# Kernel optimization log

Hardware: AMD Instinct MI355X
Metric: run time of the kernel (lower is better)

## Reference

```python
import jax, jax.numpy as jnp
import numpy as np

B, T, V = 32, 100, 20000
E, H, M, DD = 128, 128, 64, 2


def setup_inputs() -> dict:
    key = jax.random.key(0)
    ks = jax.random.split(key, 12)
    x = jax.random.uniform(ks[0], (B, T, V), dtype=jnp.float32)
    # zero out trailing timesteps per example so Masking layer matters
    lens = jax.random.randint(ks[1], (B,), T * 3 // 4, T + 1)
    tmask = (jnp.arange(T)[None, :] < lens[:, None]).astype(jnp.float32)
    x = x * tmask[:, :, None]
    a = jax.random.uniform(ks[2], (B, V), dtype=jnp.float32)
    d = jax.random.normal(ks[3], (B, DD), dtype=jnp.float32)
    # parameters
    emb = jax.random.uniform(ks[4], (V, E), minval=-0.1, maxval=0.1, dtype=jnp.float32)
    s = 1.0 / np.sqrt(E)
    gru_k = jax.random.uniform(ks[5], (E, 3 * H), minval=-s, maxval=s, dtype=jnp.float32)
    gru_rk = jax.random.normal(ks[6], (H, 3 * H), dtype=jnp.float32) / np.sqrt(H)
    gru_b_i = jnp.zeros((3 * H,), jnp.float32)   # input bias (reset_after=True)
    gru_b_r = jnp.zeros((3 * H,), jnp.float32)   # recurrent bias
    s1 = 1.0 / np.sqrt(H + E)
    W1 = jax.random.uniform(ks[7], (H + E, M), minval=-s1, maxval=s1, dtype=jnp.float32)
    b1 = jnp.zeros((M,), jnp.float32)
    s2 = 1.0 / np.sqrt(M + DD)
    W2 = jax.random.uniform(ks[8], (M + DD, 1), minval=-s2, maxval=s2, dtype=jnp.float32)
    b2 = jnp.zeros((1,), jnp.float32)
    return dict(x=x, a=a, d=d, emb=emb, gru_k=gru_k, gru_rk=gru_rk,
                gru_b_i=gru_b_i, gru_b_r=gru_b_r, W1=W1, b1=b1, W2=W2, b2=b2)


def _gru_final_state(xe, mask, gru_k, gru_rk, gru_b_i, gru_b_r):
    # xe: [B,T,E], mask: [B,T] bool. Keras GRU, reset_after=True, eval mode (dropout off).
    Hn = gru_rk.shape[0]
    x_proj = jnp.einsum('bte,eh->bth', xe, gru_k) + gru_b_i  # [B,T,3H]

    def step(h, inp):
        xp_t, m_t = inp                      # [B,3H], [B]
        rec = h @ gru_rk + gru_b_r           # [B,3H]
        xz, xr, xh = jnp.split(xp_t, 3, axis=-1)
        rz, rr, rh = jnp.split(rec, 3, axis=-1)
        z = jax.nn.sigmoid(xz + rz)
        r = jax.nn.sigmoid(xr + rr)
        hh = jnp.tanh(xh + r * rh)
        h_new = z * h + (1.0 - z) * hh
        h = jnp.where(m_t[:, None], h_new, h)  # masked steps carry state
        return h, None

    h0 = jnp.zeros((xe.shape[0], Hn), xe.dtype)
    h_final, _ = jax.lax.scan(step, h0, (jnp.swapaxes(x_proj, 0, 1), jnp.swapaxes(mask, 0, 1)))
    return h_final


def reference(x, a, d, emb, gru_k, gru_rk, gru_b_i, gru_b_r, W1, b1, W2, b2):
    ae = jnp.tanh(a @ emb)                       # [B,E]
    xe = jnp.tanh(jnp.einsum('btv,ve->bte', x, emb))  # [B,T,E]
    mask = jnp.any(xe != 0.0, axis=-1)           # Masking(mask_value=0.0)
    h = _gru_final_state(xe, mask, gru_k, gru_rk, gru_b_i, gru_b_r)  # [B,H]
    c = jnp.tanh(jnp.concatenate([h, ae], axis=1) @ W1 + b1)         # [B,M]
    out = jax.nn.sigmoid(jnp.concatenate([c, d], axis=1) @ W2 + b2)  # [B,1]
    return out
```

## Files before the change

kernel.cpp:

```cpp
#include <hip/hip_runtime.h>

typedef __attribute__((ext_vector_type(8))) short short8;
typedef __attribute__((ext_vector_type(4))) float float4v;

#define V_ 20000
#define KS 8
#define ARS 264

__device__ __forceinline__ unsigned short f2bf(float f) {
    union { float f; unsigned int u; } v; v.f = f;
    unsigned int u = v.u;
    u += 0x7fffu + ((u >> 16) & 1u);
    return (unsigned short)(u >> 16);
}

__device__ __forceinline__ float fast_tanh(float x) {
    float xc = fminf(15.f, fmaxf(-15.f, x));
    float e = __expf(2.f * xc);
    return (e - 1.f) / (e + 1.f);
}

__device__ __forceinline__ float sigmoidf_(float x) {
    float xc = fminf(30.f, fmaxf(-30.f, x));
    return 1.f / (1.f + __expf(-xc));
}

__global__ __launch_bounds__(256) void cvt_embT(const float* __restrict__ emb,
                                                unsigned short* __restrict__ embT) {
    __shared__ unsigned short tile[128 * 65];
    int tid = threadIdx.x;
    int k0 = blockIdx.x * 64;
    const float4v* e4 = (const float4v*)emb;
    #pragma unroll
    for (int c = 0; c < 8; ++c) {
        int l4 = c * 256 + tid;
        int k = l4 >> 5;
        int n4 = l4 & 31;
        float4v f = {0.f, 0.f, 0.f, 0.f};
        if (k0 + k < V_) f = e4[(size_t)(k0 + k) * 32 + n4];
        tile[(n4 * 4 + 0) * 65 + k] = f2bf(f.x);
        tile[(n4 * 4 + 1) * 65 + k] = f2bf(f.y);
        tile[(n4 * 4 + 2) * 65 + k] = f2bf(f.z);
        tile[(n4 * 4 + 3) * 65 + k] = f2bf(f.w);
    }
    __syncthreads();
    #pragma unroll
    for (int c = 0; c < 4; ++c) {
        int l8 = c * 256 + tid;
        int n = l8 >> 3, seg = l8 & 7;
        int kk = k0 + seg * 8;
        if (kk < V_) {
            short8 v;
            #pragma unroll
            for (int i = 0; i < 8; ++i) v[i] = (short)tile[n * 65 + seg * 8 + i];
            *(short8*)(embT + (size_t)n * V_ + kk) = v;
        }
    }
}

__global__ __launch_bounds__(256) void big_gemm(const float* __restrict__ x,
                                                const float* __restrict__ a,
                                                const unsigned short* __restrict__ embT,
                                                float* __restrict__ partial) {
    __shared__ unsigned short Alds[2][16 * ARS];
    int tid = threadIdx.x;
    int bx = blockIdx.x, by = blockIdx.y;
    int m0 = bx * 16;
    const int per = 79 / KS, extra = 79 % KS;
    int sc0 = by * per + (by < extra ? by : extra);
    int nsc = per + (by < extra ? 1 : 0);

    int r = tid >> 4, c = tid & 15;
    int rg = m0 + r;
    const float* __restrict__ srcA = (rg < 3200) ? (x + (size_t)rg * V_)
                                                 : (a + (size_t)(rg - 3200) * V_);
    int lane = tid & 63, w = tid >> 6;
    int ln = lane & 15, quad = lane >> 4;
    const unsigned short* __restrict__ bb0 = embT + (size_t)(w * 32 + ln) * V_ + quad * 8;
    const unsigned short* __restrict__ bb1 = bb0 + (size_t)16 * V_;
    int aoff = ln * ARS + quad * 8;

    float4v acc0 = {0.f, 0.f, 0.f, 0.f}, acc1 = {0.f, 0.f, 0.f, 0.f};
    float4v p0, p1, p2, p3;

    {
        int k0 = sc0 * 256;
        int nkb = 625 - sc0 * 8; if (nkb > 8) nkb = 8;
        int L = nkb * 32;
        if (c * 16 < L) {
            const float4v* ap = (const float4v*)(srcA + k0 + c * 16);
            p0 = ap[0]; p1 = ap[1]; p2 = ap[2]; p3 = ap[3];
        } else {
            p0 = p1 = p2 = p3 = (float4v){0.f, 0.f, 0.f, 0.f};
        }
        short8 w0, w1;
        w0[0]=(short)f2bf(p0.x); w0[1]=(short)f2bf(p0.y); w0[2]=(short)f2bf(p0.z); w0[3]=(short)f2bf(p0.w);
        w0[4]=(short)f2bf(p1.x); w0[5]=(short)f2bf(p1.y); w0[6]=(short)f2bf(p1.z); w0[7]=(short)f2bf(p1.w);
        w1[0]=(short)f2bf(p2.x); w1[1]=(short)f2bf(p2.y); w1[2]=(short)f2bf(p2.z); w1[3]=(short)f2bf(p2.w);
        w1[4]=(short)f2bf(p3.x); w1[5]=(short)f2bf(p3.y); w1[6]=(short)f2bf(p3.z); w1[7]=(short)f2bf(p3.w);
        *(short8*)&Alds[0][r * ARS + c * 16]     = w0;
        *(short8*)&Alds[0][r * ARS + c * 16 + 8] = w1;
    }
    __syncthreads();

    for (int s = 0; s < nsc; ++s) {
        int buf = s & 1;
        int sc = sc0 + s;
        int k0 = sc * 256;
        int nkb = 625 - sc * 8; if (nkb > 8) nkb = 8;
        bool more = (s + 1 < nsc);
        if (more) {
            int k0n = (sc + 1) * 256;
            int nkbn = 625 - (sc + 1) * 8; if (nkbn > 8) nkbn = 8;
            if (c * 16 < nkbn * 32) {
                const float4v* ap = (const float4v*)(srcA + k0n + c * 16);
                p0 = ap[0]; p1 = ap[1]; p2 = ap[2]; p3 = ap[3];
            } else {
                p0 = p1 = p2 = p3 = (float4v){0.f, 0.f, 0.f, 0.f};
            }
        }
        const unsigned short* bp0 = bb0 + k0;
        const unsigned short* bp1 = bb1 + k0;
        const unsigned short* al = &Alds[buf][aoff];
        if (nkb == 8) {
            #pragma unroll
            for (int kk = 0; kk < 8; ++kk) {
                short8 af = *(const short8*)(al + kk * 32);
                short8 f0 = *(const short8*)(bp0 + kk * 32);
                short8 f1 = *(const short8*)(bp1 + kk * 32);
                acc0 = __builtin_amdgcn_mfma_f32_16x16x32_bf16(af, f0, acc0, 0, 0, 0);
                acc1 = __builtin_amdgcn_mfma_f32_16x16x32_bf16(af, f1, acc1, 0, 0, 0);
            }
        } else {
            for (int kk = 0; kk < nkb; ++kk) {
                short8 af = *(const short8*)(al + kk * 32);
                short8 f0 = *(const short8*)(bp0 + kk * 32);
                short8 f1 = *(const short8*)(bp1 + kk * 32);
                acc0 = __builtin_amdgcn_mfma_f32_16x16x32_bf16(af, f0, acc0, 0, 0, 0);
                acc1 = __builtin_amdgcn_mfma_f32_16x16x32_bf16(af, f1, acc1, 0, 0, 0);
            }
        }
        if (more) {
            int nxt = buf ^ 1;
            short8 w0, w1;
            w0[0]=(short)f2bf(p0.x); w0[1]=(short)f2bf(p0.y); w0[2]=(short)f2bf(p0.z); w0[3]=(short)f2bf(p0.w);
            w0[4]=(short)f2bf(p1.x); w0[5]=(short)f2bf(p1.y); w0[6]=(short)f2bf(p1.z); w0[7]=(short)f2bf(p1.w);
            w1[0]=(short)f2bf(p2.x); w1[1]=(short)f2bf(p2.y); w1[2]=(short)f2bf(p2.z); w1[3]=(short)f2bf(p2.w);
            w1[4]=(short)f2bf(p3.x); w1[5]=(short)f2bf(p3.y); w1[6]=(short)f2bf(p3.z); w1[7]=(short)f2bf(p3.w);
            *(short8*)&Alds[nxt][r * ARS + c * 16]     = w0;
            *(short8*)&Alds[nxt][r * ARS + c * 16 + 8] = w1;
        }
        __syncthreads();
    }

    size_t base = ((size_t)by * 3232 + m0 + quad * 4) * 128 + w * 32 + ln;
    #pragma unroll
    for (int reg = 0; reg < 4; ++reg) {
        partial[base + (size_t)reg * 128]      = acc0[reg];
        partial[base + (size_t)reg * 128 + 16] = acc1[reg];
    }
}

__global__ __launch_bounds__(128) void reduce_tanh(const float* __restrict__ partial,
                                                   float* __restrict__ xe,
                                                   float* __restrict__ ae,
                                                   float* __restrict__ maskg) {
    int row = blockIdx.x;
    int e = threadIdx.x;
    float s = 0.f;
    #pragma unroll
    for (int k = 0; k < KS; ++k)
        s += partial[((size_t)k * 3232 + row) * 128 + e];
    float v = fast_tanh(s);
    if (row < 3200) {
        xe[(size_t)row * 128 + e] = v;
        __shared__ int any;
        if (e == 0) any = 0;
        __syncthreads();
        if (v != 0.f) any = 1;
        __syncthreads();
        if (e == 0) maskg[row] = any ? 1.f : 0.f;
    } else {
        ae[(row - 3200) * 128 + e] = v;
    }
}

__global__ __launch_bounds__(384) void xproj_kernel(const float* __restrict__ xe,
                                                    const float* __restrict__ gru_k,
                                                    const float* __restrict__ b_i,
                                                    float* __restrict__ xproj) {
    __shared__ float xs[16 * 128];
    int tid = threadIdx.x;
    int row0 = blockIdx.x * 16;
    const float4v* src = (const float4v*)(xe + (size_t)row0 * 128);
    float4v* dstl = (float4v*)xs;
    #pragma unroll
    for (int c = 0; c < 2; ++c) {
        int i4 = c * 384 + tid;
        if (i4 < 512) dstl[i4] = src[i4];
    }
    __syncthreads();
    int j = tid;
    float acc[16];
    #pragma unroll
    for (int r = 0; r < 16; ++r) acc[r] = 0.f;
    float bi = b_i[j];
    for (int k4 = 0; k4 < 32; ++k4) {
        float g0 = gru_k[(k4 * 4 + 0) * 384 + j];
        float g1 = gru_k[(k4 * 4 + 1) * 384 + j];
        float g2 = gru_k[(k4 * 4 + 2) * 384 + j];
        float g3 = gru_k[(k4 * 4 + 3) * 384 + j];
        #pragma unroll
        for (int r = 0; r < 16; ++r) {
            float4v xv = *(const float4v*)&xs[r * 128 + k4 * 4];
            acc[r] = fmaf(xv.x, g0, acc[r]);
            acc[r] = fmaf(xv.y, g1, acc[r]);
            acc[r] = fmaf(xv.z, g2, acc[r]);
            acc[r] = fmaf(xv.w, g3, acc[r]);
        }
    }
    #pragma unroll
    for (int r = 0; r < 16; ++r)
        xproj[(size_t)(row0 + r) * 384 + j] = acc[r] + bi;
}

__global__ __launch_bounds__(384) void gru_kernel(const float* __restrict__ xproj,
                                                  const float* __restrict__ maskg,
                                                  const float* __restrict__ gru_rk,
                                                  const float* __restrict__ b_r,
                                                  float* __restrict__ hout) {
    int b = blockIdx.x;
    int j = threadIdx.x;
    float w[128];
    #pragma unroll
    for (int k = 0; k < 128; ++k) w[k] = gru_rk[k * 384 + j];
    float br = b_r[j];
    __shared__ float4v hs4[32];
    __shared__ float recs[384];
    float* hs = (float*)hs4;
    float hreg = 0.f;
    if (j < 128) hs[j] = 0.f;
    const float* xp_base = xproj + (size_t)b * 100 * 384;
    const float* mk = maskg + b * 100;
    float xz = 0.f, xr = 0.f, xh = 0.f;
    if (j < 128) { xz = xp_base[j]; xr = xp_base[128 + j]; xh = xp_base[256 + j]; }
    __syncthreads();
    for (int t = 0; t < 100; ++t) {
        float nxz = 0.f, nxr = 0.f, nxh = 0.f;
        if (t < 99 && j < 128) {
            const float* nb = xp_base + (t + 1) * 384;
            nxz = nb[j]; nxr = nb[128 + j]; nxh = nb[256 + j];
        }
        float s0 = 0.f, s1 = 0.f, s2 = 0.f, s3 = 0.f;
        #pragma unroll
        for (int k4 = 0; k4 < 32; ++k4) {
            float4v hv = hs4[k4];
            s0 = fmaf(hv.x, w[k4 * 4 + 0], s0);
            s1 = fmaf(hv.y, w[k4 * 4 + 1], s1);
            s2 = fmaf(hv.z, w[k4 * 4 + 2], s2);
            s3 = fmaf(hv.w, w[k4 * 4 + 3], s3);
        }
        recs[j] = br + ((s0 + s1) + (s2 + s3));
        __syncthreads();
        if (j < 128) {
            float z = sigmoidf_(xz + recs[j]);
            float r = sigmoidf_(xr + recs[128 + j]);
            float hh = fast_tanh(xh + r * recs[256 + j]);
            float hn = z * hreg + (1.f - z) * hh;
            hreg = (mk[t] != 0.f) ? hn : hreg;
            hs[j] = hreg;
        }
        __syncthreads();
        xz = nxz; xr = nxr; xh = nxh;
    }
    if (j < 128) hout[b * 128 + j] = hreg;
}

__global__ __launch_bounds__(64) void head_kernel(const float* __restrict__ hout,
                                                  const float* __restrict__ ae,
                                                  const float* __restrict__ d,
                                                  const float* __restrict__ W1,
                                                  const float* __restrict__ b1,
                                                  const float* __restrict__ W2,
                                                  const float* __restrict__ b2,
                                                  float* __restrict__ out) {
    int b = blockIdx.x;
    int m = threadIdx.x;
    float s = b1[m];
    const float* hb = hout + b * 128;
    const float* ab = ae + b * 128;
    #pragma unroll 4
    for (int k = 0; k < 128; ++k) s = fmaf(hb[k], W1[k * 64 + m], s);
    #pragma unroll 4
    for (int k = 0; k < 128; ++k) s = fmaf(ab[k], W1[(128 + k) * 64 + m], s);
    float c = fast_tanh(s);
    float p = c * W2[m];
    #pragma unroll
    for (int off = 32; off > 0; off >>= 1) p += __shfl_down(p, off);
    if (m == 0) {
        p += d[b * 2 + 0] * W2[64] + d[b * 2 + 1] * W2[65] + b2[0];
        out[b] = sigmoidf_(p);
    }
}

extern "C" void kernel_launch(void* const* d_in, const int* in_sizes, int n_in,
                              void* d_out, int out_size, void* d_ws, size_t ws_size,
                              hipStream_t stream) {
    (void)in_sizes; (void)n_in; (void)out_size; (void)ws_size;
    const float* x      = (const float*)d_in[0];
    const float* a      = (const float*)d_in[1];
    const float* d      = (const float*)d_in[2];
    const float* emb    = (const float*)d_in[3];
    const float* gru_k  = (const float*)d_in[4];
    const float* gru_rk = (const float*)d_in[5];
    const float* gbi    = (const float*)d_in[6];
    const float* gbr    = (const float*)d_in[7];
    const float* W1     = (const float*)d_in[8];
    const float* b1     = (const float*)d_in[9];
    const float* W2     = (const float*)d_in[10];
    const float* b2     = (const float*)d_in[11];
    float* out = (float*)d_out;

    char* ws = (char*)d_ws;
    unsigned short* embT = (unsigned short*)(ws);
    float* xe      = (float*)(ws + 5120000);
    float* ae      = (float*)(ws + 6758400);
    float* maskg   = (float*)(ws + 6774784);
    float* xproj   = (float*)(ws + 6787584);
    float* hout    = (float*)(ws + 11702784);
    float* partial = (float*)(ws + 11719168);

    hipLaunchKernelGGL(cvt_embT,    dim3(313),      dim3(256), 0, stream, emb, embT);
    hipLaunchKernelGGL(big_gemm,    dim3(202, KS),  dim3(256), 0, stream, x, a, embT, partial);
    hipLaunchKernelGGL(reduce_tanh, dim3(3232),     dim3(128), 0, stream, partial, xe, ae, maskg);
    hipLaunchKernelGGL(xproj_kernel,dim3(200),      dim3(384), 0, stream, xe, gru_k, gbi, xproj);
    hipLaunchKernelGGL(gru_kernel,  dim3(32),       dim3(384), 0, stream, xproj, maskg, gru_rk, gbr, hout);
    hipLaunchKernelGGL(head_kernel, dim3(32),       dim3(64),  0, stream, hout, ae, d, W1, b1, W2, b2, out);
}
```

Baseline: 601.3 us.

## Restructure embedding GEMM to per-wave 32x128 register tiles with 32-way split-K

Rewrites big_gemm so each wave owns a 32-row by 128-column output tile. The wave loads its fp32 activation rows straight from global memory into registers, converts them to bf16, and reuses them across eight B fragments. This removes the LDS staging and the block-wide barriers, and cuts redundant re-reads of the transposed embedding across blocks. Split-K rises from 8 to 32 to keep enough waves in flight. The cost is a partial buffer four times larger, which the reduction kernel has to write and read, and a risk of overflowing the workspace if it was sized for 8 slices.

```diff
diff --git a/kernel.cpp b/kernel.cpp
--- a/kernel.cpp
+++ b/kernel.cpp
@@ -4,8 +4,7 @@
 typedef __attribute__((ext_vector_type(4))) float float4v;
 
 #define V_ 20000
-#define KS 8
-#define ARS 264
+#define KS 32
 
 __device__ __forceinline__ unsigned short f2bf(float f) {
     union { float f; unsigned int u; } v; v.f = f;
@@ -58,106 +57,80 @@
     }
 }
 
-__global__ __launch_bounds__(256) void big_gemm(const float* __restrict__ x,
-                                                const float* __restrict__ a,
-                                                const unsigned short* __restrict__ embT,
-                                                float* __restrict__ partial) {
-    __shared__ unsigned short Alds[2][16 * ARS];
+__global__ __launch_bounds__(256, 3) void big_gemm(const float* __restrict__ x,
+                                                   const float* __restrict__ a,
+                                                   const unsigned short* __restrict__ embT,
+                                                   float* __restrict__ partial) {
     int tid = threadIdx.x;
-    int bx = blockIdx.x, by = blockIdx.y;
-    int m0 = bx * 16;
-    const int per = 79 / KS, extra = 79 % KS;
-    int sc0 = by * per + (by < extra ? by : extra);
-    int nsc = per + (by < extra ? 1 : 0);
-
-    int r = tid >> 4, c = tid & 15;
-    int rg = m0 + r;
-    const float* __restrict__ srcA = (rg < 3200) ? (x + (size_t)rg * V_)
-                                                 : (a + (size_t)(rg - 3200) * V_);
-    int lane = tid & 63, w = tid >> 6;
+    int w = tid >> 6, lane = tid & 63;
     int ln = lane & 15, quad = lane >> 4;
-    const unsigned short* __restrict__ bb0 = embT + (size_t)(w * 32 + ln) * V_ + quad * 8;
-    const unsigned short* __restrict__ bb1 = bb0 + (size_t)16 * V_;
-    int aoff = ln * ARS + quad * 8;
-
-    float4v acc0 = {0.f, 0.f, 0.f, 0.f}, acc1 = {0.f, 0.f, 0.f, 0.f};
-    float4v p0, p1, p2, p3;
-
-    {
-        int k0 = sc0 * 256;
-        int nkb = 625 - sc0 * 8; if (nkb > 8) nkb = 8;
-        int L = nkb * 32;
-        if (c * 16 < L) {
-            const float4v* ap = (const float4v*)(srcA + k0 + c * 16);
-            p0 = ap[0]; p1 = ap[1]; p2 = ap[2]; p3 = ap[3];
-        } else {
-            p0 = p1 = p2 = p3 = (float4v){0.f, 0.f, 0.f, 0.f};
-        }
-        short8 w0, w1;
-        w0[0]=(short)f2bf(p0.x); w0[1]=(short)f2bf(p0.y); w0[2]=(short)f2bf(p0.z); w0[3]=(short)f2bf(p0.w);
-        w0[4]=(short)f2bf(p1.x); w0[5]=(short)f2bf(p1.y); w0[6]=(short)f2bf(p1.z); w0[7]=(short)f2bf(p1.w);
-        w1[0]=(short)f2bf(p2.x); w1[1]=(short)f2bf(p2.y); w1[2]=(short)f2bf(p2.z); w1[3]=(short)f2bf(p2.w);
-        w1[4]=(short)f2bf(p3.x); w1[5]=(short)f2bf(p3.y); w1[6]=(short)f2bf(p3.z); w1[7]=(short)f2bf(p3.w);
-        *(short8*)&Alds[0][r * ARS + c * 16]     = w0;
-        *(short8*)&Alds[0][r * ARS + c * 16 + 8] = w1;
-    }
-    __syncthreads();
-
-    for (int s = 0; s < nsc; ++s) {
-        int buf = s & 1;
-        int sc = sc0 + s;
-        int k0 = sc * 256;
-        int nkb = 625 - sc * 8; if (nkb > 8) nkb = 8;
-        bool more = (s + 1 < nsc);
-        if (more) {
-            int k0n = (sc + 1) * 256;
-            int nkbn = 625 - (sc + 1) * 8; if (nkbn > 8) nkbn = 8;
-            if (c * 16 < nkbn * 32) {
-                const float4v* ap = (const float4v*)(srcA + k0n + c * 16);
-                p0 = ap[0]; p1 = ap[1]; p2 = ap[2]; p3 = ap[3];
-            } else {
-                p0 = p1 = p2 = p3 = (float4v){0.f, 0.f, 0.f, 0.f};
-            }
-        }
-        const unsigned short* bp0 = bb0 + k0;
-        const unsigned short* bp1 = bb1 + k0;
-        const unsigned short* al = &Alds[buf][aoff];
-        if (nkb == 8) {
+    int tile = blockIdx.x * 4 + w;
+    if (tile > 100) return;
+    int by = blockIdx.y;
+    int r0 = tile * 32;
+
+    int kb0 = by * 19 + (by < 17 ? by : 17);
+    int cnt = 19 + (by < 17 ? 1 : 0);
+
+    const float* __restrict__ src0;
+    const float* __restrict__ src1;
+    if (r0 < 3200) {
+        src0 = x + (size_t)(r0 + ln) * V_;
+        src1 = x + (size_t)(r0 + 16 + ln) * V_;
+    } else {
+        src0 = a + (size_t)ln * V_;
+        src1 = a + (size_t)(16 + ln) * V_;
+    }
+    const unsigned short* __restrict__ bp0 = embT + (size_t)ln * V_ + quad * 8;
+
+    float4v acc[2][8];
+    #pragma unroll
+    for (int f = 0; f < 2; ++f)
+        #pragma unroll
+        for (int t = 0; t < 8; ++t) acc[f][t] = (float4v){0.f, 0.f, 0.f, 0.f};
+
+    int kq = kb0 * 32 + quad * 8;
+    float4v a00 = *(const float4v*)(src0 + kq);
+    float4v a01 = *(const float4v*)(src0 + kq + 4);
+    float4v a10 = *(const float4v*)(src1 + kq);
+    float4v a11 = *(const float4v*)(src1 + kq + 4);
+
+    for (int s = 0; s < cnt; ++s) {
+        int k = (kb0 + s) * 32;
+        float4v n00, n01, n10, n11;
+        if (s + 1 < cnt) {
+            int knq = k + 32 + quad * 8;
+            n00 = *(const float4v*)(src0 + knq);
+            n01 = *(const float4v*)(src0 + knq + 4);
+            n10 = *(const float4v*)(src1 + knq);
+            n11 = *(const float4v*)(src1 + knq + 4);
+        }
+        short8 bf[8];
+        #pragma unroll
+        for (int t = 0; t < 8; ++t)
+            bf[t] = *(const short8*)(bp0 + (size_t)t * 16 * V_ + k);
+        short8 pa0, pa1;
+        pa0[0]=(short)f2bf(a00.x); pa0[1]=(short)f2bf(a00.y); pa0[2]=(short)f2bf(a00.z); pa0[3]=(short)f2bf(a00.w);
+        pa0[4]=(short)f2bf(a01.x); pa0[5]=(short)f2bf(a01.y); pa0[6]=(short)f2bf(a01.z); pa0[7]=(short)f2bf(a01.w);
+        pa1[0]=(short)f2bf(a10.x); pa1[1]=(short)f2bf(a10.y); pa1[2]=(short)f2bf(a10.z); pa1[3]=(short)f2bf(a10.w);
+        pa1[4]=(short)f2bf(a11.x); pa1[5]=(short)f2bf(a11.y); pa1[6]=(short)f2bf(a11.z); pa1[7]=(short)f2bf(a11.w);
+        #pragma unroll
+        for (int t = 0; t < 8; ++t) {
+            acc[0][t] = __builtin_amdgcn_mfma_f32_16x16x32_bf16(pa0, bf[t], acc[0][t], 0, 0, 0);
+            acc[1][t] = __builtin_amdgcn_mfma_f32_16x16x32_bf16(pa1, bf[t], acc[1][t], 0, 0, 0);
+        }
+        a00 = n00; a01 = n01; a10 = n10; a11 = n11;
+    }
+
+    float* dst = partial + ((size_t)by * 3232 + r0 + quad * 4) * 128 + ln;
+    #pragma unroll
+    for (int f = 0; f < 2; ++f) {
+        #pragma unroll
+        for (int t = 0; t < 8; ++t) {
             #pragma unroll
-            for (int kk = 0; kk < 8; ++kk) {
-                short8 af = *(const short8*)(al + kk * 32);
-                short8 f0 = *(const short8*)(bp0 + kk * 32);
-                short8 f1 = *(const short8*)(bp1 + kk * 32);
-                acc0 = __builtin_amdgcn_mfma_f32_16x16x32_bf16(af, f0, acc0, 0, 0, 0);
-                acc1 = __builtin_amdgcn_mfma_f32_16x16x32_bf16(af, f1, acc1, 0, 0, 0);
-            }
-        } else {
-            for (int kk = 0; kk < nkb; ++kk) {
-                short8 af = *(const short8*)(al + kk * 32);
-                short8 f0 = *(const short8*)(bp0 + kk * 32);
-                short8 f1 = *(const short8*)(bp1 + kk * 32);
-                acc0 = __builtin_amdgcn_mfma_f32_16x16x32_bf16(af, f0, acc0, 0, 0, 0);
-                acc1 = __builtin_amdgcn_mfma_f32_16x16x32_bf16(af, f1, acc1, 0, 0, 0);
-            }
-        }
-        if (more) {
-            int nxt = buf ^ 1;
-            short8 w0, w1;
-            w0[0]=(short)f2bf(p0.x); w0[1]=(short)f2bf(p0.y); w0[2]=(short)f2bf(p0.z); w0[3]=(short)f2bf(p0.w);
-            w0[4]=(short)f2bf(p1.x); w0[5]=(short)f2bf(p1.y); w0[6]=(short)f2bf(p1.z); w0[7]=(short)f2bf(p1.w);
-            w1[0]=(short)f2bf(p2.x); w1[1]=(short)f2bf(p2.y); w1[2]=(short)f2bf(p2.z); w1[3]=(short)f2bf(p2.w);
-            w1[4]=(short)f2bf(p3.x); w1[5]=(short)f2bf(p3.y); w1[6]=(short)f2bf(p3.z); w1[7]=(short)f2bf(p3.w);
-            *(short8*)&Alds[nxt][r * ARS + c * 16]     = w0;
-            *(short8*)&Alds[nxt][r * ARS + c * 16 + 8] = w1;
-        }
-        __syncthreads();
-    }
-
-    size_t base = ((size_t)by * 3232 + m0 + quad * 4) * 128 + w * 32 + ln;
-    #pragma unroll
-    for (int reg = 0; reg < 4; ++reg) {
-        partial[base + (size_t)reg * 128]      = acc0[reg];
-        partial[base + (size_t)reg * 128 + 16] = acc1[reg];
+            for (int reg = 0; reg < 4; ++reg)
+                dst[(size_t)(f * 16 + reg) * 128 + t * 16] = acc[f][t][reg];
+        }
     }
 }
 
@@ -331,7 +304,7 @@
     float* partial = (float*)(ws + 11719168);
 
     hipLaunchKernelGGL(cvt_embT,    dim3(313),      dim3(256), 0, stream, emb, embT);
-    hipLaunchKernelGGL(big_gemm,    dim3(202, KS),  dim3(256), 0, stream, x, a, embT, partial);
+    hipLaunchKernelGGL(big_gemm,    dim3(26, KS),   dim3(256), 0, stream, x, a, embT, partial);
     hipLaunchKernelGGL(reduce_tanh, dim3(3232),     dim3(128), 0, stream, partial, xe, ae, maskg);
     hipLaunchKernelGGL(xproj_kernel,dim3(200),      dim3(384), 0, stream, xe, gru_k, gbi, xproj);
     hipLaunchKernelGGL(gru_kernel,  dim3(32),       dim3(384), 0, stream, xproj, maskg, gru_rk, gbr, hout);
```

Result: no change. 605.9 us (+0.8%).
